# Performance work log

Hardware: AMD Instinct MI355X
Metric: run time of the kernel (lower is better)

Reference implementation:

```python
import jax, jax.numpy as jnp
import numpy as np


def setup_inputs() -> dict:
    key = jax.random.key(0)
    ks = jax.random.split(key, 5)
    B, in_ch, H, W = 8, 256, 128, 128
    C = in_ch // 4
    x = jax.random.normal(ks[0], (B, in_ch, H, W), dtype=jnp.float32)
    # 1x1 conv weights stored as [out_ch, in_ch] (kernel spatial dims are 1)
    w_in = jax.random.normal(ks[1], (C, in_ch), dtype=jnp.float32) * (1.0 / np.sqrt(in_ch))
    b_in = jax.random.normal(ks[2], (C,), dtype=jnp.float32) * 0.01
    w_out = jax.random.normal(ks[3], (in_ch, C), dtype=jnp.float32) * (1.0 / np.sqrt(C))
    b_out = jax.random.normal(ks[4], (in_ch,), dtype=jnp.float32) * 0.01
    detal = jnp.array([0.1], dtype=jnp.float32)
    return {"x": x, "w_in": w_in, "b_in": b_in, "w_out": w_out, "b_out": b_out, "detal": detal}


def _mda(x, w_in, b_in, w_out, b_out, detal):
    # InConv: 1x1 conv == channel GEMM
    inp = jnp.einsum('bihw,oi->bohw', x, w_in) + b_in[None, :, None, None]
    B, C, H, W = inp.shape

    # ---- W branch ----
    # AdaptiveAvgPool2d((None,1)) -> mean over W; softmax over size-1 axis (== ones, kept for faithfulness)
    f_w = jax.nn.softmax(inp.mean(axis=3, keepdims=True), axis=3)          # [B,C,H,1]
    f_w = jnp.transpose(f_w, (0, 3, 1, 2)).reshape(B, C * H, 1)
    Xw = inp.reshape(B, C * H, W)
    Gw = Xw * f_w                                                          # [B,CH,W]
    Tw = jax.nn.softmax(jnp.einsum('bkw,bkv->bwv', Gw, Gw), axis=1)        # [B,W,W], softmax over rows
    Wo = jnp.einsum('bkw,bwv->bkv', Xw, Tw).reshape(B, C, H, W)

    # ---- H branch ----
    f_h = jax.nn.softmax(jnp.transpose(inp, (0, 1, 3, 2)).mean(axis=3, keepdims=True), axis=3)  # [B,C,W,1]
    f_h = jnp.transpose(f_h, (0, 3, 1, 2)).reshape(B, C * W, 1)
    Xh = inp.reshape(B, C * W, H)  # raw .view as in torch (scrambles H/W axes intentionally)
    Gh = Xh * f_h
    Th = jax.nn.softmax(jnp.einsum('bkh,bkg->bhg', Gh, Gh), axis=1)        # [B,H,H]
    Ho = jnp.einsum('bkh,bhg->bkg', Xh, Th).reshape(B, C, H, W)

    # ---- C branch ----
    perm = jnp.transpose(inp, (0, 2, 3, 1))                                # [B,H,W,C]
    f_c = jax.nn.softmax(perm.mean(axis=3, keepdims=True), axis=3)         # [B,H,W,1]
    f_c = jnp.transpose(f_c, (0, 3, 1, 2)).reshape(B, H * W, 1)
    Xc = perm.reshape(B, H * W, C)
    Gc = f_c * Xc
    Tc = jax.nn.softmax(jnp.einsum('bnc,bnd->bcd', Gc, Gc), axis=1)        # [B,C,C]
    # torch does .view(B,C,H,W) on a [B,H*W,C] tensor: raw reshape, NOT a transpose
    Co = jnp.einsum('bnc,bcd->bnd', Xc, Tc).reshape(B, C, H, W)

    s = detal[0] * (Co + Wo + Ho)
    # OuConv 1x1 + residual
    return jnp.einsum('bchw,oc->bohw', s, w_out) + b_out[None, :, None, None] + x


def reference(x, w_in, b_in, w_out, b_out, detal):
    return _mda(x, w_in, b_in, w_out, b_out, detal)
```

## Files before the change

### kernel.cpp

```cpp
#include <hip/hip_runtime.h>
#include <math.h>

#define NB 8
#define IC 256
#define CC 64
#define HH 128
#define WW 128
#define NN (HH*WW)
#define NKW 64
#define NKC 64

static constexpr size_t SZ_INP  = (size_t)NB * CC * NN;
static constexpr size_t OFF_INP = 0;
static constexpr size_t OFF_S   = OFF_INP + SZ_INP;
static constexpr size_t OFF_PC  = OFF_S + SZ_INP;
static constexpr size_t OFF_TW  = OFF_PC + (size_t)NB * NKC * 4096;
static constexpr size_t OFF_TC  = OFF_TW + (size_t)NB * 16384;
static constexpr size_t OFF_WT  = OFF_TC + (size_t)NB * 4096;
static constexpr size_t OFF_WOT = OFF_WT + 16384;

__global__ __launch_bounds__(256) void k_wt(
    const float* __restrict__ w_in, const float* __restrict__ w_out,
    float* __restrict__ w_in_t, float* __restrict__ w_out_t)
{
    const int idx = blockIdx.x * 256 + threadIdx.x;
    if (idx < 16384) {
        const int o = idx & 63, i = idx >> 6;
        w_in_t[idx] = w_in[o * IC + i];
    } else {
        const int j = idx - 16384;
        const int o = j & 255, c = j >> 8;
        w_out_t[j] = w_out[o * CC + c];
    }
}

__global__ __launch_bounds__(256) void k_inconv(
    const float* __restrict__ x, const float* __restrict__ wt,
    const float* __restrict__ b_in, float* __restrict__ inp)
{
    __shared__ float xs[16 * 260];
    __shared__ float wl[16 * 68];
    const int b  = blockIdx.y;
    const int n0 = blockIdx.x * 256;
    const int t  = threadIdx.x;
    const int og = t >> 5;
    const int ng = t & 31;

    const int sr = t >> 4, sc = (t & 15) * 4;
    const float* xbase = x + ((size_t)b * IC + sr) * NN + n0 + sc;
    const float* wbase = wt + (size_t)sr * 64 + sc;
    float* xdst = xs + sr * 260 + sc;
    float* wdst = wl + sr * 68 + sc;

    float acc[8][8];
#pragma unroll
    for (int p = 0; p < 8; p++)
#pragma unroll
        for (int q = 0; q < 8; q++) acc[p][q] = 0.f;

    for (int i0 = 0; i0 < IC; i0 += 16) {
        __syncthreads();
        {
            const float* xsrc = xbase + (size_t)i0 * NN;
            const float4 a0 = *(const float4*)(xsrc);
            const float4 a1 = *(const float4*)(xsrc + 64);
            const float4 a2 = *(const float4*)(xsrc + 128);
            const float4 a3 = *(const float4*)(xsrc + 192);
            const float4 w0 = *(const float4*)(wbase + (size_t)i0 * 64);
            *(float4*)(xdst)       = a0;
            *(float4*)(xdst + 64)  = a1;
            *(float4*)(xdst + 128) = a2;
            *(float4*)(xdst + 192) = a3;
            *(float4*)(wdst)       = w0;
        }
        __syncthreads();
#pragma unroll 4
        for (int i = 0; i < 16; ++i) {
            const float4 wa = *(const float4*)(wl + i * 68 + og * 8);
            const float4 wb = *(const float4*)(wl + i * 68 + og * 8 + 4);
            const float4 xa = *(const float4*)(xs + i * 260 + ng * 4);
            const float4 xb = *(const float4*)(xs + i * 260 + 128 + ng * 4);
            const float wv[8] = {wa.x, wa.y, wa.z, wa.w, wb.x, wb.y, wb.z, wb.w};
            const float xv[8] = {xa.x, xa.y, xa.z, xa.w, xb.x, xb.y, xb.z, xb.w};
#pragma unroll
            for (int p = 0; p < 8; p++)
#pragma unroll
                for (int q = 0; q < 8; q++) acc[p][q] += wv[p] * xv[q];
        }
    }
#pragma unroll
    for (int p = 0; p < 8; ++p) {
        const int oo = og * 8 + p;
        const float bo = b_in[oo];
        float* base = inp + ((size_t)b * CC + oo) * NN + n0;
        *(float4*)(base + ng * 4) =
            make_float4(acc[p][0] + bo, acc[p][1] + bo, acc[p][2] + bo, acc[p][3] + bo);
        *(float4*)(base + 128 + ng * 4) =
            make_float4(acc[p][4] + bo, acc[p][5] + bo, acc[p][6] + bo, acc[p][7] + bo);
    }
}

__global__ __launch_bounds__(256) void k_gramW(const float* __restrict__ inp, float* __restrict__ pW)
{
    __shared__ float xs[8 * 128];
    const int b = blockIdx.y, kc = blockIdx.x;
    const int t = threadIdx.x, tx = t & 15, ty = t >> 4;
    const float* Xb = inp + (size_t)b * CC * NN;
    const int k0 = kc * ((CC * HH) / NKW);

    float acc[8][8];
#pragma unroll
    for (int i = 0; i < 8; i++)
#pragma unroll
        for (int j = 0; j < 8; j++) acc[i][j] = 0.f;

    for (int kk = k0; kk < k0 + (CC * HH) / NKW; kk += 8) {
        __syncthreads();
        for (int idx = t; idx < 1024; idx += 256)
            xs[idx] = Xb[((size_t)kk + (idx >> 7)) * WW + (idx & 127)];
        __syncthreads();
#pragma unroll
        for (int k = 0; k < 8; k++) {
            const float* row = xs + k * 128;
            float4 t0 = *(const float4*)(row + ty * 8);
            float4 t1 = *(const float4*)(row + ty * 8 + 4);
            float4 u0 = *(const float4*)(row + tx * 8);
            float4 u1 = *(const float4*)(row + tx * 8 + 4);
            float av[8] = {t0.x, t0.y, t0.z, t0.w, t1.x, t1.y, t1.z, t1.w};
            float bv[8] = {u0.x, u0.y, u0.z, u0.w, u1.x, u1.y, u1.z, u1.w};
#pragma unroll
            for (int i = 0; i < 8; i++)
#pragma unroll
                for (int j = 0; j < 8; j++) acc[i][j] += av[i] * bv[j];
        }
    }
    float* dst = pW + ((size_t)b * NKW + kc) * 16384;
#pragma unroll
    for (int i = 0; i < 8; i++)
#pragma unroll
        for (int j = 0; j < 8; j += 4) {
            float4 v = make_float4(acc[i][j], acc[i][j + 1], acc[i][j + 2], acc[i][j + 3]);
            *(float4*)(dst + (ty * 8 + i) * 128 + tx * 8 + j) = v;
        }
}

__global__ __launch_bounds__(256) void k_redW(const float* __restrict__ pW, float* __restrict__ Tw)
{
    const int b = blockIdx.y;
    const int idx = blockIdx.x * 256 + threadIdx.x;
    const float* p = pW + (size_t)b * NKW * 16384 + idx;
    float acc = 0.f;
#pragma unroll
    for (int k = 0; k < NKW; k++) acc += p[(size_t)k * 16384];
    Tw[(size_t)b * 16384 + idx] = acc;
}

__global__ __launch_bounds__(1024) void k_softW(float* __restrict__ Tw)
{
    __shared__ float red[32 * 33];
    const int b = blockIdx.x, v0 = blockIdx.y * 32;
    const int t = threadIdx.x;
    const int vc = t & 31, wg = t >> 5;
    float* S = Tw + (size_t)b * 16384 + v0 + vc;

    float v[4];
    float m = -3.4e38f;
#pragma unroll
    for (int j = 0; j < 4; j++) { v[j] = S[(wg * 4 + j) * 128]; m = fmaxf(m, v[j]); }
    red[wg * 33 + vc] = m;
    __syncthreads();
    for (int st = 16; st > 0; st >>= 1) {
        if (wg < st) red[wg * 33 + vc] = fmaxf(red[wg * 33 + vc], red[(wg + st) * 33 + vc]);
        __syncthreads();
    }
    m = red[vc];
    __syncthreads();
    float sum = 0.f;
#pragma unroll
    for (int j = 0; j < 4; j++) { v[j] = __expf(v[j] - m); sum += v[j]; }
    red[wg * 33 + vc] = sum;
    __syncthreads();
    for (int st = 16; st > 0; st >>= 1) {
        if (wg < st) red[wg * 33 + vc] += red[(wg + st) * 33 + vc];
        __syncthreads();
    }
    const float inv = 1.f / red[vc];
#pragma unroll
    for (int j = 0; j < 4; j++) S[(wg * 4 + j) * 128] = v[j] * inv;
}

__global__ __launch_bounds__(256) void k_gramC(const float* __restrict__ inp, float* __restrict__ pC)
{
    __shared__ float xt[32 * 68];
    const int b = blockIdx.y, nc = blockIdx.x;
    const int t = threadIdx.x, tx = t & 15, ty = t >> 4;
    const float* ip = inp + (size_t)b * CC * NN;
    const int n0 = nc * (NN / NKC);

    float acc[4][4];
#pragma unroll
    for (int i = 0; i < 4; i++)
#pragma unroll
        for (int j = 0; j < 4; j++) acc[i][j] = 0.f;

    const int scc = t >> 2;
    const int sn  = (t & 3) * 8;

    for (int nt = 0; nt < NN / NKC; nt += 32) {
        __syncthreads();
        {
            const float* src = ip + (size_t)scc * NN + n0 + nt + sn;
            float v[8];
            *(float4*)(v)     = *(const float4*)(src);
            *(float4*)(v + 4) = *(const float4*)(src + 4);
#pragma unroll
            for (int j = 0; j < 8; j++) xt[(sn + j) * 68 + scc] = v[j];
        }
        __syncthreads();
#pragma unroll 8
        for (int nn = 0; nn < 32; nn++) {
            const float4 a4 = *(const float4*)(xt + nn * 68 + ty * 4);
            const float4 e4 = *(const float4*)(xt + nn * 68 + tx * 4);
            const float av[4] = {a4.x, a4.y, a4.z, a4.w};
            const float ev[4] = {e4.x, e4.y, e4.z, e4.w};
#pragma unroll
            for (int i = 0; i < 4; i++)
#pragma unroll
                for (int j = 0; j < 4; j++) acc[i][j] += av[i] * ev[j];
        }
    }
    float* dst = pC + ((size_t)b * NKC + nc) * 4096;
#pragma unroll
    for (int i = 0; i < 4; i++) {
        float4 v = make_float4(acc[i][0], acc[i][1], acc[i][2], acc[i][3]);
        *(float4*)(dst + (ty * 4 + i) * 64 + tx * 4) = v;
    }
}

__global__ __launch_bounds__(256) void k_redC(const float* __restrict__ pC, float* __restrict__ Tc)
{
    const int b = blockIdx.y;
    const int idx = blockIdx.x * 256 + threadIdx.x;
    const float* p = pC + (size_t)b * NKC * 4096 + idx;
    float acc = 0.f;
#pragma unroll
    for (int k = 0; k < NKC; k++) acc += p[(size_t)k * 4096];
    Tc[(size_t)b * 4096 + idx] = acc;
}

__global__ __launch_bounds__(1024) void k_softC(float* __restrict__ Tc)
{
    __shared__ float red[16 * 65];
    const int b = blockIdx.x;
    const int t = threadIdx.x;
    const int dc = t & 63, cg = t >> 6;
    float* S = Tc + (size_t)b * 4096 + dc;

    float v[4];
    float m = -3.4e38f;
#pragma unroll
    for (int j = 0; j < 4; j++) { v[j] = S[(cg * 4 + j) * 64]; m = fmaxf(m, v[j]); }
    red[cg * 65 + dc] = m;
    __syncthreads();
    for (int st = 8; st > 0; st >>= 1) {
        if (cg < st) red[cg * 65 + dc] = fmaxf(red[cg * 65 + dc], red[(cg + st) * 65 + dc]);
        __syncthreads();
    }
    m = red[dc];
    __syncthreads();
    float sum = 0.f;
#pragma unroll
    for (int j = 0; j < 4; j++) { v[j] = __expf(v[j] - m); sum += v[j]; }
    red[cg * 65 + dc] = sum;
    __syncthreads();
    for (int st = 8; st > 0; st >>= 1) {
        if (cg < st) red[cg * 65 + dc] += red[(cg + st) * 65 + dc];
        __syncthreads();
    }
    const float inv = 1.f / red[dc];
#pragma unroll
    for (int j = 0; j < 4; j++) S[(cg * 4 + j) * 64] = v[j] * inv;
}

__global__ __launch_bounds__(256) void k_co(
    const float* __restrict__ inp, const float* __restrict__ Tc,
    const float* __restrict__ detal, float* __restrict__ s)
{
    __shared__ float tc[64 * 68];
    __shared__ float xs[64 * 132];
    const int b  = blockIdx.y;
    const int n0 = blockIdx.x * 128;
    const int t  = threadIdx.x;
    const int d4 = (t & 15) * 4;
    const int g8 = (t >> 4) * 8;

    {
        const int sr = t >> 2, sc = (t & 3) * 4;
        const float* src = inp + ((size_t)b * CC + sr) * NN + n0;
        float* dst = xs + sr * 132;
#pragma unroll
        for (int k = 0; k < 8; k++)
            *(float4*)(dst + sc + 16 * k) = *(const float4*)(src + sc + 16 * k);
        const float* tsrc = Tc + (size_t)b * 4096 + sr * 64;
        float* tdst = tc + sr * 68;
#pragma unroll
        for (int k = 0; k < 4; k++)
            *(float4*)(tdst + sc + 16 * k) = *(const float4*)(tsrc + sc + 16 * k);
    }
    __syncthreads();

    float acc[8][4];
#pragma unroll
    for (int i = 0; i < 8; i++)
#pragma unroll
        for (int j = 0; j < 4; j++) acc[i][j] = 0.f;

#pragma unroll 4
    for (int c = 0; c < 64; c++) {
        const float4 t4 = *(const float4*)(tc + c * 68 + d4);
        const float4 xa = *(const float4*)(xs + c * 132 + g8);
        const float4 xb = *(const float4*)(xs + c * 132 + g8 + 4);
        const float xv[8] = {xa.x, xa.y, xa.z, xa.w, xb.x, xb.y, xb.z, xb.w};
        const float tv[4] = {t4.x, t4.y, t4.z, t4.w};
#pragma unroll
        for (int i = 0; i < 8; i++)
#pragma unroll
            for (int j = 0; j < 4; j++) acc[i][j] += xv[i] * tv[j];
    }
    const float scl = detal[0];
    float* sb = s + (size_t)b * CC * NN + (size_t)n0 * 64;
#pragma unroll
    for (int i = 0; i < 8; i++) {
        float4 v = make_float4(acc[i][0] * scl, acc[i][1] * scl,
                               acc[i][2] * scl, acc[i][3] * scl);
        *(float4*)(sb + (size_t)(g8 + i) * 64 + d4) = v;
    }
}

__global__ __launch_bounds__(256, 2) void k_wo(
    const float* __restrict__ inp, const float* __restrict__ Tw,
    const float* __restrict__ detal, float* __restrict__ s)
{
    __shared__ float xt[32 * 132];
    __shared__ float twl[32 * 132];
    const int b = blockIdx.y, c = blockIdx.x;
    const int t = threadIdx.x;
    const int rg = t >> 4;
    const int vg = t & 15;

    const float* ip = inp + ((size_t)b * CC + c) * NN;
    const float* twg = Tw + (size_t)b * 16384;

    float acc[8][8];
#pragma unroll
    for (int p = 0; p < 8; p++)
#pragma unroll
        for (int q = 0; q < 8; q++) acc[p][q] = 0.f;

    for (int w0 = 0; w0 < 128; w0 += 32) {
        __syncthreads();
        {
            const int h = t >> 1, wq = (t & 1) * 16;
            const float* src = ip + (size_t)h * WW + w0 + wq;
            float v[16];
            *(float4*)(v)      = *(const float4*)(src);
            *(float4*)(v + 4)  = *(const float4*)(src + 4);
            *(float4*)(v + 8)  = *(const float4*)(src + 8);
            *(float4*)(v + 12) = *(const float4*)(src + 12);
#pragma unroll
            for (int j = 0; j < 16; j++) xt[(wq + j) * 132 + h] = v[j];
        }
        {
            const int w = t >> 3, cq = (t & 7) * 16;
            const float* src = twg + (size_t)(w0 + w) * 128 + cq;
            float* dst = twl + w * 132 + cq;
#pragma unroll
            for (int k = 0; k < 4; k++)
                *(float4*)(dst + 4 * k) = *(const float4*)(src + 4 * k);
        }
        __syncthreads();
#pragma unroll 4
        for (int w = 0; w < 32; ++w) {
            const float4 ra = *(const float4*)(xt + w * 132 + rg * 8);
            const float4 rb = *(const float4*)(xt + w * 132 + rg * 8 + 4);
            const float4 ta = *(const float4*)(twl + w * 132 + vg * 4);
            const float4 tb = *(const float4*)(twl + w * 132 + 64 + vg * 4);
            const float rv[8] = {ra.x, ra.y, ra.z, ra.w, rb.x, rb.y, rb.z, rb.w};
            const float tv[8] = {ta.x, ta.y, ta.z, ta.w, tb.x, tb.y, tb.z, tb.w};
#pragma unroll
            for (int p = 0; p < 8; p++)
#pragma unroll
                for (int q = 0; q < 8; q++) acc[p][q] += rv[p] * tv[q];
        }
    }

    const float sc2 = 2.0f * detal[0];
    float* sp = s + ((size_t)b * CC + c) * NN;
#pragma unroll
    for (int p = 0; p < 8; ++p) {
        const int h = rg * 8 + p;
        float* q0 = sp + (size_t)h * WW + vg * 4;
        float* q1 = sp + (size_t)h * WW + 64 + vg * 4;
        float4 c0 = *(const float4*)q0;
        float4 c1 = *(const float4*)q1;
        c0.x += sc2 * acc[p][0]; c0.y += sc2 * acc[p][1];
        c0.z += sc2 * acc[p][2]; c0.w += sc2 * acc[p][3];
        c1.x += sc2 * acc[p][4]; c1.y += sc2 * acc[p][5];
        c1.z += sc2 * acc[p][6]; c1.w += sc2 * acc[p][7];
        *(float4*)q0 = c0;
        *(float4*)q1 = c1;
    }
}

__global__ __launch_bounds__(256) void k_outconv(
    const float* __restrict__ s, const float* __restrict__ wot,
    const float* __restrict__ b_out, const float* __restrict__ x,
    float* __restrict__ outp)
{
    __shared__ float ss[16 * 260];
    __shared__ float wl[16 * 68];
    const int b  = blockIdx.z;
    const int o0 = blockIdx.y * 64;
    const int n0 = blockIdx.x * 256;
    const int t  = threadIdx.x;
    const int og = t >> 5;
    const int ng = t & 31;

    const int sr = t >> 4, sc = (t & 15) * 4;
    const float* sbase = s + ((size_t)b * CC + sr) * NN + n0 + sc;
    const float* wbase = wot + (size_t)sr * IC + o0 + sc;
    float* sdst = ss + sr * 260 + sc;
    float* wdst = wl + sr * 68 + sc;

    float acc[8][8];
#pragma unroll
    for (int p = 0; p < 8; p++)
#pragma unroll
        for (int q = 0; q < 8; q++) acc[p][q] = 0.f;

    for (int c0 = 0; c0 < CC; c0 += 16) {
        __syncthreads();
        {
            const float* ssrc = sbase + (size_t)c0 * NN;
            const float4 a0 = *(const float4*)(ssrc);
            const float4 a1 = *(const float4*)(ssrc + 64);
            const float4 a2 = *(const float4*)(ssrc + 128);
            const float4 a3 = *(const float4*)(ssrc + 192);
            const float4 w0 = *(const float4*)(wbase + (size_t)c0 * IC);
            *(float4*)(sdst)       = a0;
            *(float4*)(sdst + 64)  = a1;
            *(float4*)(sdst + 128) = a2;
            *(float4*)(sdst + 192) = a3;
            *(float4*)(wdst)       = w0;
        }
        __syncthreads();
#pragma unroll 4
        for (int c = 0; c < 16; ++c) {
            const float4 wa = *(const float4*)(wl + c * 68 + og * 8);
            const float4 wb = *(const float4*)(wl + c * 68 + og * 8 + 4);
            const float4 sa = *(const float4*)(ss + c * 260 + ng * 4);
            const float4 sb = *(const float4*)(ss + c * 260 + 128 + ng * 4);
            const float wv[8] = {wa.x, wa.y, wa.z, wa.w, wb.x, wb.y, wb.z, wb.w};
            const float sv[8] = {sa.x, sa.y, sa.z, sa.w, sb.x, sb.y, sb.z, sb.w};
#pragma unroll
            for (int p = 0; p < 8; p++)
#pragma unroll
                for (int q = 0; q < 8; q++) acc[p][q] += wv[p] * sv[q];
        }
    }

#pragma unroll
    for (int p = 0; p < 8; ++p) {
        const int oo = o0 + og * 8 + p;
        const float bo = b_out[oo];
        const float* xb = x + ((size_t)b * IC + oo) * NN + n0;
        float* ob = outp + ((size_t)b * IC + oo) * NN + n0;
        const float4 x0 = *(const float4*)(xb + ng * 4);
        const float4 x1 = *(const float4*)(xb + 128 + ng * 4);
        *(float4*)(ob + ng * 4) =
            make_float4(acc[p][0] + bo + x0.x, acc[p][1] + bo + x0.y,
                        acc[p][2] + bo + x0.z, acc[p][3] + bo + x0.w);
        *(float4*)(ob + 128 + ng * 4) =
            make_float4(acc[p][4] + bo + x1.x, acc[p][5] + bo + x1.y,
                        acc[p][6] + bo + x1.z, acc[p][7] + bo + x1.w);
    }
}

extern "C" void kernel_launch(void* const* d_in, const int* in_sizes, int n_in,
                              void* d_out, int out_size, void* d_ws, size_t ws_size,
                              hipStream_t stream)
{
    const float* x     = (const float*)d_in[0];
    const float* w_in  = (const float*)d_in[1];
    const float* b_in  = (const float*)d_in[2];
    const float* w_out = (const float*)d_in[3];
    const float* b_out = (const float*)d_in[4];
    const float* detal = (const float*)d_in[5];
    float* out = (float*)d_out;

    float* ws   = (float*)d_ws;
    float* inp  = ws + OFF_INP;
    float* s    = ws + OFF_S;
    float* pW   = ws + OFF_S;
    float* pC   = ws + OFF_PC;
    float* Tw   = ws + OFF_TW;
    float* Tc   = ws + OFF_TC;
    float* wt   = ws + OFF_WT;
    float* wot  = ws + OFF_WOT;

    k_wt     <<<dim3(128),              256, 0, stream>>>(w_in, w_out, wt, wot);
    k_inconv <<<dim3(NN / 256, NB),     256, 0, stream>>>(x, wt, b_in, inp);
    k_gramW  <<<dim3(NKW, NB),          256, 0, stream>>>(inp, pW);
    k_redW   <<<dim3(64, NB),           256, 0, stream>>>(pW, Tw);
    k_softW  <<<dim3(NB, 4),           1024, 0, stream>>>(Tw);
    k_gramC  <<<dim3(NKC, NB),          256, 0, stream>>>(inp, pC);
    k_redC   <<<dim3(16, NB),           256, 0, stream>>>(pC, Tc);
    k_softC  <<<dim3(NB),              1024, 0, stream>>>(Tc);
    k_co     <<<dim3(NN / 128, NB),     256, 0, stream>>>(inp, Tc, detal, s);
    k_wo     <<<dim3(CC, NB),           256, 0, stream>>>(inp, Tw, detal, s);
    k_outconv<<<dim3(NN / 256, 4, NB),  256, 0, stream>>>(s, wot, b_out, x, out);
}
```

Measured before the change: 445.8 us.

## Retile Gram-W, Wo and output-conv kernels for larger staging and reuse

k_gramW now stages 32 rows per sync with float4 loads into a padded shared tile, replacing 8-row scalar loads, so it issues fewer barriers and wider global reads. k_wo is split across two H halves with 128-thread blocks, giving more blocks and smaller shared tiles. k_outconv now covers all 256 output channels per block over 64 spatial positions, so each s element is read once instead of four times, at the cost of fewer, larger blocks and more shared memory for weights.

Measured after the change: 444.4 us. About the same (-0.3%).

```diff
diff --git a/kernel.cpp b/kernel.cpp
--- a/kernel.cpp
+++ b/kernel.cpp
@@ -102,7 +102,7 @@
 
 __global__ __launch_bounds__(256) void k_gramW(const float* __restrict__ inp, float* __restrict__ pW)
 {
-    __shared__ float xs[8 * 128];
+    __shared__ float xs[32 * 132];
     const int b = blockIdx.y, kc = blockIdx.x;
     const int t = threadIdx.x, tx = t & 15, ty = t >> 4;
     const float* Xb = inp + (size_t)b * CC * NN;
@@ -114,14 +114,20 @@
 #pragma unroll
         for (int j = 0; j < 8; j++) acc[i][j] = 0.f;
 
-    for (int kk = k0; kk < k0 + (CC * HH) / NKW; kk += 8) {
-        __syncthreads();
-        for (int idx = t; idx < 1024; idx += 256)
-            xs[idx] = Xb[((size_t)kk + (idx >> 7)) * WW + (idx & 127)];
-        __syncthreads();
-#pragma unroll
-        for (int k = 0; k < 8; k++) {
-            const float* row = xs + k * 128;
+    for (int kk = k0; kk < k0 + (CC * HH) / NKW; kk += 32) {
+        __syncthreads();
+        {
+            const int r = t >> 3, cq = (t & 7) * 16;
+            const float* src = Xb + ((size_t)kk + r) * WW + cq;
+            float* dst = xs + r * 132 + cq;
+#pragma unroll
+            for (int j = 0; j < 4; j++)
+                *(float4*)(dst + 4 * j) = *(const float4*)(src + 4 * j);
+        }
+        __syncthreads();
+#pragma unroll 8
+        for (int k = 0; k < 32; k++) {
+            const float* row = xs + k * 132;
             float4 t0 = *(const float4*)(row + ty * 8);
             float4 t1 = *(const float4*)(row + ty * 8 + 4);
             float4 u0 = *(const float4*)(row + tx * 8);
@@ -337,18 +343,19 @@
     }
 }
 
-__global__ __launch_bounds__(256, 2) void k_wo(
+__global__ __launch_bounds__(128) void k_wo(
     const float* __restrict__ inp, const float* __restrict__ Tw,
     const float* __restrict__ detal, float* __restrict__ s)
 {
-    __shared__ float xt[32 * 132];
+    __shared__ float xt[32 * 68];
     __shared__ float twl[32 * 132];
-    const int b = blockIdx.y, c = blockIdx.x;
+    const int b = blockIdx.z, hc = blockIdx.y, c = blockIdx.x;
     const int t = threadIdx.x;
     const int rg = t >> 4;
     const int vg = t & 15;
-
-    const float* ip = inp + ((size_t)b * CC + c) * NN;
+    const int h0 = hc * 64;
+
+    const float* ip = inp + ((size_t)b * CC + c) * NN + (size_t)h0 * WW;
     const float* twg = Tw + (size_t)b * 16384;
 
     float acc[8][8];
@@ -368,21 +375,21 @@
             *(float4*)(v + 8)  = *(const float4*)(src + 8);
             *(float4*)(v + 12) = *(const float4*)(src + 12);
 #pragma unroll
-            for (int j = 0; j < 16; j++) xt[(wq + j) * 132 + h] = v[j];
+            for (int j = 0; j < 16; j++) xt[(wq + j) * 68 + h] = v[j];
         }
         {
-            const int w = t >> 3, cq = (t & 7) * 16;
+            const int w = t >> 2, cq = (t & 3) * 32;
             const float* src = twg + (size_t)(w0 + w) * 128 + cq;
             float* dst = twl + w * 132 + cq;
 #pragma unroll
-            for (int k = 0; k < 4; k++)
+            for (int k = 0; k < 8; k++)
                 *(float4*)(dst + 4 * k) = *(const float4*)(src + 4 * k);
         }
         __syncthreads();
 #pragma unroll 4
         for (int w = 0; w < 32; ++w) {
-            const float4 ra = *(const float4*)(xt + w * 132 + rg * 8);
-            const float4 rb = *(const float4*)(xt + w * 132 + rg * 8 + 4);
+            const float4 ra = *(const float4*)(xt + w * 68 + rg * 8);
+            const float4 rb = *(const float4*)(xt + w * 68 + rg * 8 + 4);
             const float4 ta = *(const float4*)(twl + w * 132 + vg * 4);
             const float4 tb = *(const float4*)(twl + w * 132 + 64 + vg * 4);
             const float rv[8] = {ra.x, ra.y, ra.z, ra.w, rb.x, rb.y, rb.z, rb.w};
@@ -395,7 +402,7 @@
     }
 
     const float sc2 = 2.0f * detal[0];
-    float* sp = s + ((size_t)b * CC + c) * NN;
+    float* sp = s + ((size_t)b * CC + c) * NN + (size_t)h0 * WW;
 #pragma unroll
     for (int p = 0; p < 8; ++p) {
         const int h = rg * 8 + p;
@@ -417,20 +424,21 @@
     const float* __restrict__ b_out, const float* __restrict__ x,
     float* __restrict__ outp)
 {
-    __shared__ float ss[16 * 260];
-    __shared__ float wl[16 * 68];
-    const int b  = blockIdx.z;
-    const int o0 = blockIdx.y * 64;
-    const int n0 = blockIdx.x * 256;
+    __shared__ float ss[16 * 68];
+    __shared__ float wl[16 * 260];
+    const int b  = blockIdx.y;
+    const int n0 = blockIdx.x * 64;
     const int t  = threadIdx.x;
-    const int og = t >> 5;
-    const int ng = t & 31;
-
-    const int sr = t >> 4, sc = (t & 15) * 4;
-    const float* sbase = s + ((size_t)b * CC + sr) * NN + n0 + sc;
-    const float* wbase = wot + (size_t)sr * IC + o0 + sc;
-    float* sdst = ss + sr * 260 + sc;
-    float* wdst = wl + sr * 68 + sc;
+    const int og = t >> 3;
+    const int ng = t & 7;
+
+    const int sr = t >> 4;
+    const int sq = (t & 15) * 4;
+    const int wq = (t & 15) * 16;
+    const float* sbase = s + ((size_t)b * CC + sr) * NN + n0 + sq;
+    const float* wbase = wot + (size_t)sr * IC + wq;
+    float* sdst = ss + sr * 68 + sq;
+    float* wdst = wl + sr * 260 + wq;
 
     float acc[8][8];
 #pragma unroll
@@ -441,25 +449,25 @@
     for (int c0 = 0; c0 < CC; c0 += 16) {
         __syncthreads();
         {
-            const float* ssrc = sbase + (size_t)c0 * NN;
-            const float4 a0 = *(const float4*)(ssrc);
-            const float4 a1 = *(const float4*)(ssrc + 64);
-            const float4 a2 = *(const float4*)(ssrc + 128);
-            const float4 a3 = *(const float4*)(ssrc + 192);
-            const float4 w0 = *(const float4*)(wbase + (size_t)c0 * IC);
-            *(float4*)(sdst)       = a0;
-            *(float4*)(sdst + 64)  = a1;
-            *(float4*)(sdst + 128) = a2;
-            *(float4*)(sdst + 192) = a3;
-            *(float4*)(wdst)       = w0;
+            const float4 a0 = *(const float4*)(sbase + (size_t)c0 * NN);
+            const float* wsrc = wbase + (size_t)c0 * IC;
+            const float4 w0 = *(const float4*)(wsrc);
+            const float4 w1 = *(const float4*)(wsrc + 4);
+            const float4 w2 = *(const float4*)(wsrc + 8);
+            const float4 w3 = *(const float4*)(wsrc + 12);
+            *(float4*)(sdst)      = a0;
+            *(float4*)(wdst)      = w0;
+            *(float4*)(wdst + 4)  = w1;
+            *(float4*)(wdst + 8)  = w2;
+            *(float4*)(wdst + 12) = w3;
         }
         __syncthreads();
 #pragma unroll 4
         for (int c = 0; c < 16; ++c) {
-            const float4 wa = *(const float4*)(wl + c * 68 + og * 8);
-            const float4 wb = *(const float4*)(wl + c * 68 + og * 8 + 4);
-            const float4 sa = *(const float4*)(ss + c * 260 + ng * 4);
-            const float4 sb = *(const float4*)(ss + c * 260 + 128 + ng * 4);
+            const float4 wa = *(const float4*)(wl + c * 260 + og * 8);
+            const float4 wb = *(const float4*)(wl + c * 260 + og * 8 + 4);
+            const float4 sa = *(const float4*)(ss + c * 68 + ng * 4);
+            const float4 sb = *(const float4*)(ss + c * 68 + 32 + ng * 4);
             const float wv[8] = {wa.x, wa.y, wa.z, wa.w, wb.x, wb.y, wb.z, wb.w};
             const float sv[8] = {sa.x, sa.y, sa.z, sa.w, sb.x, sb.y, sb.z, sb.w};
 #pragma unroll
@@ -471,16 +479,16 @@
 
 #pragma unroll
     for (int p = 0; p < 8; ++p) {
-        const int oo = o0 + og * 8 + p;
+        const int oo = og * 8 + p;
         const float bo = b_out[oo];
         const float* xb = x + ((size_t)b * IC + oo) * NN + n0;
         float* ob = outp + ((size_t)b * IC + oo) * NN + n0;
         const float4 x0 = *(const float4*)(xb + ng * 4);
-        const float4 x1 = *(const float4*)(xb + 128 + ng * 4);
+        const float4 x1 = *(const float4*)(xb + 32 + ng * 4);
         *(float4*)(ob + ng * 4) =
             make_float4(acc[p][0] + bo + x0.x, acc[p][1] + bo + x0.y,
                         acc[p][2] + bo + x0.z, acc[p][3] + bo + x0.w);
-        *(float4*)(ob + 128 + ng * 4) =
+        *(float4*)(ob + 32 + ng * 4) =
             make_float4(acc[p][4] + bo + x1.x, acc[p][5] + bo + x1.y,
                         acc[p][6] + bo + x1.z, acc[p][7] + bo + x1.w);
     }
@@ -517,6 +525,6 @@
     k_redC   <<<dim3(16, NB),           256, 0, stream>>>(pC, Tc);
     k_softC  <<<dim3(NB),              1024, 0, stream>>>(Tc);
     k_co     <<<dim3(NN / 128, NB),     256, 0, stream>>>(inp, Tc, detal, s);
-    k_wo     <<<dim3(CC, NB),           256, 0, stream>>>(inp, Tw, detal, s);
-    k_outconv<<<dim3(NN / 256, 4, NB),  256, 0, stream>>>(s, wot, b_out, x, out);
-}
+    k_wo     <<<dim3(CC, 2, NB),        128, 0, stream>>>(inp, Tw, detal, s);
+    k_outconv<<<dim3(NN / 64, NB),      256, 0, stream>>>(s, wot, b_out, x, out);
+}
```
